# Performance work log

Hardware: AMD Instinct MI355X
Metric: run time of the kernel (lower is better)

## Reference

```python
import jax, jax.numpy as jnp
import numpy as np

VAR0, VAR1 = 0.1, 0.2   # cfg['variance']
THRESH = 0.5            # overlap_thresh
THETA = 0.01
NEGPOS = 3


def decode(loc, priors):
    # priors center-form [P,4]; returns point-form boxes [P,4]
    cxcy = priors[:, :2] + loc[:, :2] * VAR0 * priors[:, 2:]
    wh = priors[:, 2:] * jnp.exp(loc[:, 2:] * VAR1)
    return jnp.concatenate([cxcy - wh * 0.5, cxcy + wh * 0.5], axis=1)


def center_size(b):
    return jnp.concatenate([(b[:, :2] + b[:, 2:]) * 0.5, b[:, 2:] - b[:, :2]], axis=1)


def encode(matched, priors_c):
    # matched point-form [P,4], priors_c center-form [P,4]
    g_cxcy = ((matched[:, :2] + matched[:, 2:]) * 0.5 - priors_c[:, :2]) / (VAR0 * priors_c[:, 2:])
    g_wh = jnp.log((matched[:, 2:] - matched[:, :2]) / priors_c[:, 2:]) / VAR1
    return jnp.concatenate([g_cxcy, g_wh], axis=1)


def jaccard(a, b):
    # a [G,4], b [P,4] point form -> IoU [G,P]
    lt = jnp.maximum(a[:, None, :2], b[None, :, :2])
    rb = jnp.minimum(a[:, None, 2:], b[None, :, 2:])
    wh = jnp.clip(rb - lt, 0.0)
    inter = wh[..., 0] * wh[..., 1]
    area_a = ((a[:, 2] - a[:, 0]) * (a[:, 3] - a[:, 1]))[:, None]
    area_b = ((b[:, 2] - b[:, 0]) * (b[:, 3] - b[:, 1]))[None, :]
    return inter / (area_a + area_b - inter)


def _match_one(truths, labels, gt_mask, arm_loc, priors):
    # refine_match with arm_loc (use_ARM=True path)
    P = priors.shape[0]
    G = truths.shape[0]
    dec = decode(arm_loc, priors)                                 # [P,4]
    ov = jnp.where(gt_mask[:, None], jaccard(truths, dec), -1.0)  # [G,P], padded GT masked out
    best_prior_idx = jnp.argmax(ov, axis=1)                       # [G]
    best_truth_ov = jnp.max(ov, axis=0)                           # [P]
    best_truth_idx = jnp.argmax(ov, axis=0)                       # [P]
    safe = jnp.where(gt_mask, best_prior_idx, P)                  # OOB index -> dropped scatter
    best_truth_ov = best_truth_ov.at[safe].set(2.0, mode='drop')  # force-match each valid GT
    best_truth_idx = best_truth_idx.at[safe].set(jnp.arange(G), mode='drop')
    matched = truths[best_truth_idx]                              # [P,4]
    conf = jnp.where(best_truth_ov < THRESH, 0, labels[best_truth_idx])
    loc = encode(matched, center_size(dec))
    return loc, conf


def forward(arm_loc, arm_conf, odm_loc, odm_conf, priors, targets, num_gts):
    B, P, C = odm_conf.shape
    truths = targets[..., :4]
    labels = targets[..., 4].astype(jnp.int32)
    gt_mask = jnp.arange(targets.shape[1])[None, :] < num_gts[:, None]
    loc_t, conf_t = jax.vmap(_match_one, in_axes=(0, 0, 0, 0, None))(
        truths, labels, gt_mask,
        jax.lax.stop_gradient(arm_loc), jax.lax.stop_gradient(priors))
    loc_t = jax.lax.stop_gradient(loc_t)    # loc_t.requires_grad = False
    conf_t = jax.lax.stop_gradient(conf_t)

    # ARM objectness filter on positives
    p_obj = jax.nn.softmax(arm_conf, axis=2)[:, :, 1]
    pos = (conf_t > 0) & (p_obj > THETA)

    # masked smooth-L1 localization loss (sum)
    posf = pos[..., None].astype(odm_loc.dtype)
    d = jnp.abs(odm_loc * posf - loc_t * posf)
    loss_l = jnp.sum(jnp.where(d < 1.0, 0.5 * d * d, d - 0.5))

    # hard negative mining on per-prior softmax loss
    batch_conf = odm_conf.reshape(-1, C)
    lc = jax.nn.logsumexp(batch_conf, axis=1) - jnp.take_along_axis(
        batch_conf, conf_t.reshape(-1, 1), axis=1)[:, 0]
    lc = jnp.where(pos.reshape(-1), 0.0, lc).reshape(B, P)
    loss_idx = jnp.argsort(-lc, axis=1)
    idx_rank = jnp.argsort(loss_idx, axis=1)
    num_pos = jnp.sum(pos.astype(jnp.int32), axis=1, keepdims=True)  # [B,1]
    num_neg = jnp.minimum(NEGPOS * num_pos, P - 1)
    neg = idx_rank < num_neg
    mask = pos | neg

    # masked cross entropy (compute on zeroed-out logits like the original, then mask)
    conf_p = (odm_conf * mask[..., None].astype(odm_conf.dtype)).reshape(-1, C)
    tgt = jnp.where(mask, conf_t, 0).reshape(-1)
    logp = jax.nn.log_softmax(conf_p, axis=1)
    ce = -jnp.take_along_axis(logp, tgt[:, None], axis=1)[:, 0]
    loss_c = jnp.sum(ce * mask.reshape(-1).astype(ce.dtype))

    N = jnp.sum(num_pos).astype(jnp.float32)
    return loss_l / N, loss_c / N


def setup_inputs():
    key = jax.random.key(0)
    ks = jax.random.split(key, 10)
    B, P, C, G = 32, 16320, 21, 40
    arm_loc = jax.random.normal(ks[0], (B, P, 4), jnp.float32) * 0.1
    arm_conf = jax.random.normal(ks[1], (B, P, 2), jnp.float32)
    odm_loc = jax.random.normal(ks[2], (B, P, 4), jnp.float32) * 0.1
    odm_conf = jax.random.normal(ks[3], (B, P, C), jnp.float32)
    # priors in center form with positive sizes
    pc = jax.random.uniform(ks[4], (P, 2), jnp.float32, 0.1, 0.9)
    pwh = jax.random.uniform(ks[5], (P, 2), jnp.float32, 0.05, 0.3)
    priors = jnp.concatenate([pc, pwh], axis=1)
    # GT boxes in point form with positive area, labels in 1..C-1, padded to G=40
    gc = jax.random.uniform(ks[6], (B, G, 2), jnp.float32, 0.2, 0.8)
    gwh = jax.random.uniform(ks[7], (B, G, 2), jnp.float32, 0.05, 0.3)
    boxes = jnp.concatenate([gc - gwh * 0.5, gc + gwh * 0.5], axis=-1)
    labels = jax.random.randint(ks[8], (B, G, 1), 1, C).astype(jnp.float32)
    targets = jnp.concatenate([boxes, labels], axis=-1)
    num_gts = jax.random.randint(ks[9], (B,), 1, G + 1).astype(jnp.int32)
    return {"arm_loc": arm_loc, "arm_conf": arm_conf, "odm_loc": odm_loc,
            "odm_conf": odm_conf, "priors": priors, "targets": targets,
            "num_gts": num_gts}


def reference(arm_loc, arm_conf, odm_loc, odm_conf, priors, targets, num_gts):
    return forward(arm_loc, arm_conf, odm_loc, odm_conf, priors, targets, num_gts)
```

## Files before the change

### kernel.cpp

```cpp
#include <hip/hip_runtime.h>
#include <math.h>

#define VAR0 0.1f
#define VAR1 0.2f
#define THRESH 0.5f
#define THETA 0.01f
#define MAXG 64
#define BLK 256
#define SELT 1024
#define NCH 16
#define NB 4096
#define CAP 2048

__device__ __forceinline__ float4 decode_box(float4 l, float4 pr) {
    float cx = pr.x + l.x * VAR0 * pr.z;
    float cy = pr.y + l.y * VAR0 * pr.w;
    float w = pr.z * expf(l.z * VAR1);
    float h = pr.w * expf(l.w * VAR1);
    return make_float4(cx - w * 0.5f, cy - h * 0.5f, cx + w * 0.5f, cy + h * 0.5f);
}

__device__ __forceinline__ float smooth_l1_sum(float4 ol, float4 t, float4 d) {
    float pcx = (d.x + d.z) * 0.5f, pcy = (d.y + d.w) * 0.5f;
    float pw = d.z - d.x, ph = d.w - d.y;
    float g0 = ((t.x + t.z) * 0.5f - pcx) / (VAR0 * pw);
    float g1 = ((t.y + t.w) * 0.5f - pcy) / (VAR0 * ph);
    float g2 = logf((t.z - t.x) / pw) / VAR1;
    float g3 = logf((t.w - t.y) / ph) / VAR1;
    float s = 0.f, dd;
    dd = fabsf(ol.x - g0); s += (dd < 1.f) ? 0.5f*dd*dd : dd - 0.5f;
    dd = fabsf(ol.y - g1); s += (dd < 1.f) ? 0.5f*dd*dd : dd - 0.5f;
    dd = fabsf(ol.z - g2); s += (dd < 1.f) ? 0.5f*dd*dd : dd - 0.5f;
    dd = fabsf(ol.w - g3); s += (dd < 1.f) ? 0.5f*dd*dd : dd - 0.5f;
    return s;
}

__device__ __forceinline__ unsigned wave_umax_bits(unsigned v) {
    int x = (int)v;
    int t;
    t = __builtin_amdgcn_update_dpp(0, x, 0x111, 0xf, 0xf, true);  x = (t > x) ? t : x;
    t = __builtin_amdgcn_update_dpp(0, x, 0x112, 0xf, 0xf, true);  x = (t > x) ? t : x;
    t = __builtin_amdgcn_update_dpp(0, x, 0x114, 0xf, 0xf, true);  x = (t > x) ? t : x;
    t = __builtin_amdgcn_update_dpp(0, x, 0x118, 0xf, 0xf, true);  x = (t > x) ? t : x;
    t = __builtin_amdgcn_update_dpp(0, x, 0x142, 0xa, 0xf, false); x = (t > x) ? t : x;
    t = __builtin_amdgcn_update_dpp(0, x, 0x143, 0xc, 0xf, false); x = (t > x) ? t : x;
    return (unsigned)__builtin_amdgcn_readlane(x, 63);
}

__global__ void k_fused(const float* __restrict__ arm_loc, const float* __restrict__ priors,
                        const float* __restrict__ arm_conf,
                        const float* __restrict__ odm_loc, const float* __restrict__ odm_conf,
                        const float* __restrict__ targets, const int* __restrict__ num_gts,
                        float* __restrict__ ce, unsigned char* __restrict__ posm,
                        unsigned* __restrict__ bb,
                        unsigned long long* __restrict__ bpw,
                        float* __restrict__ partL, int* __restrict__ partN,
                        int B, int P, int C, int G) {
    int b = blockIdx.y;
    int p0 = blockIdx.x * BLK;
    int tid = threadIdx.x;
    int p = p0 + tid;
    int lane = tid & 63, wid = tid >> 6;
    int wavebase = p0 + (tid & ~63);
    __shared__ float4 st4[MAXG];
    __shared__ float  stl[MAXG];
    __shared__ float  sarea[MAXG];
    __shared__ unsigned long long wk[4][MAXG];
    __shared__ float oc_s[BLK * 21];
    __shared__ int sng;
    if (tid == 0) sng = num_gts[b];
    for (int g = tid; g < G; g += BLK) {
        const float* tg = targets + (size_t)b * G * 5 + g * 5;
        float t0 = tg[0], t1 = tg[1], t2 = tg[2], t3 = tg[3];
        st4[g] = make_float4(t0, t1, t2, t3);
        stl[g] = tg[4];
        sarea[g] = (t2 - t0) * (t3 - t1);
    }
    int nrows = P - p0; if (nrows > BLK) nrows = BLK;
    int nf = nrows * C;
    const float* ocb = odm_conf + ((size_t)b * P + p0) * C;
    int nf4 = nf >> 2;
    const float4* ocb4 = (const float4*)ocb;
    for (int i2 = tid; i2 < nf4; i2 += BLK) ((float4*)oc_s)[i2] = ocb4[i2];
    if (tid < (nf & 3)) oc_s[(nf4 << 2) + tid] = ocb[(nf4 << 2) + tid];
    __syncthreads();
    int ng = sng;
    bool ok = p < P;
    float4 d = make_float4(0.f, 0.f, 0.f, 0.f);
    float areaB = 0.f;
    size_t i = (size_t)b * P + (ok ? p : 0);
    if (ok) {
        float4 l = ((const float4*)arm_loc)[i];
        float4 pr = ((const float4*)priors)[p];
        d = decode_box(l, pr);
        areaB = (d.z - d.x) * (d.w - d.y);
    }
    float bov = -2.0f; int bidx = 0;
    for (int g = 0; g < ng; ++g) {
        float4 t = st4[g];
        unsigned vbits = 0u;
        if (ok) {
            float lt0 = fmaxf(t.x, d.x), lt1 = fmaxf(t.y, d.y);
            float rb0 = fminf(t.z, d.z), rb1 = fminf(t.w, d.w);
            float w = rb0 - lt0; if (w < 0.f) w = 0.f;
            float h = rb1 - lt1; if (h < 0.f) h = 0.f;
            float inter = w * h;
            float ov = inter / (sarea[g] + areaB - inter);
            if (ov > bov) { bov = ov; bidx = g; }
            vbits = __float_as_uint(ov);
        }
        unsigned om = wave_umax_bits(vbits);
        unsigned long long mask = __ballot(ok && vbits == om);
        if (lane == 0) {
            unsigned long long key = 0ull;
            if (mask) {
                int p_win = wavebase + (int)__builtin_ctzll(mask);
                key = ((unsigned long long)om << 32)
                    | (unsigned long long)(0xFFFFFFFFu - (unsigned)p_win);
            }
            wk[wid][g] = key;
        }
    }
    float lsum = 0.f; int pc = 0;
    if (ok) {
        int conf_t = (bov < THRESH) ? 0 : (int)stl[bidx];
        float2 c = ((const float2*)arm_conf)[i];
        float mm = fmaxf(c.x, c.y);
        float e0 = expf(c.x - mm), e1 = expf(c.y - mm);
        float p_obj = e1 / (e0 + e1);
        bool pos = (conf_t > 0) && (p_obj > THETA);
        if (pos) {
            pc = 1;
            float4 ol = ((const float4*)odm_loc)[i];
            lsum = smooth_l1_sum(ol, st4[bidx], d);
        }
        const float* oc = oc_s + tid * C;
        float mx = oc[0];
        for (int j = 1; j < C; ++j) mx = fmaxf(mx, oc[j]);
        float sume = 0.f;
        for (int j = 0; j < C; ++j) sume += expf(oc[j] - mx);
        float lse = mx + logf(sume);
        float cev = lse - oc[conf_t];
        ce[i] = cev;
        posm[i] = pos ? 1 : 0;
        bb[i] = (__float_as_uint(bov) & 0xFFFFFFC0u) | (unsigned)bidx;
    }
    __shared__ float rl[BLK];
    __shared__ int rc[BLK];
    rl[tid] = lsum; rc[tid] = pc;
    __syncthreads();
    if (tid < ng) {
        unsigned long long k0 = wk[0][tid], k1 = wk[1][tid];
        unsigned long long k2 = wk[2][tid], k3 = wk[3][tid];
        unsigned long long m01 = k0 > k1 ? k0 : k1;
        unsigned long long m23 = k2 > k3 ? k2 : k3;
        unsigned long long m = m01 > m23 ? m01 : m23;
        bpw[(size_t)(b * G + tid) * gridDim.x + blockIdx.x] = m;
    }
    for (int off = BLK/2; off > 0; off >>= 1) {
        if (tid < off) { rl[tid] += rl[tid+off]; rc[tid] += rc[tid+off]; }
        __syncthreads();
    }
    if (tid == 0) {
        partL[b * gridDim.x + blockIdx.x] = rl[0];
        partN[b * gridDim.x + blockIdx.x] = rc[0];
    }
}

__global__ __launch_bounds__(1024) void k_fixpatch(
        const float* __restrict__ arm_loc, const float* __restrict__ priors,
        const float* __restrict__ arm_conf, const float* __restrict__ odm_loc,
        const float* __restrict__ odm_conf,
        const float* __restrict__ targets, const int* __restrict__ num_gts,
        const unsigned long long* __restrict__ bpw, const unsigned* __restrict__ bb,
        float* __restrict__ ce, unsigned char* __restrict__ posm,
        float* __restrict__ partPL, int* __restrict__ partPN,
        int B, int P, int C, int G, int NBX) {
    int b = blockIdx.x;
    int tid = threadIdx.x;
    int lane = tid & 63, wid = tid >> 6;
    __shared__ int fp[MAXG];
    __shared__ float4 st4[MAXG];
    __shared__ float  stl[MAXG];
    __shared__ int sng;
    if (tid == 0) sng = num_gts[b];
    for (int g = tid; g < G; g += 1024) {
        const float* tg = targets + (size_t)b * G * 5 + g * 5;
        st4[g] = make_float4(tg[0], tg[1], tg[2], tg[3]);
        stl[g] = tg[4];
    }
    __syncthreads();
    int ng = sng;
    for (int g = wid; g < ng; g += 16) {
        const unsigned long long* src = bpw + (size_t)(b * G + g) * NBX;
        unsigned long long key = 0ull;
        for (int j = lane; j < NBX; j += 64) {
            unsigned long long v = src[j];
            if (v > key) key = v;
        }
        for (int off = 32; off > 0; off >>= 1) {
            unsigned long long o = __shfl_down(key, (unsigned)off, 64);
            if (o > key) key = o;
        }
        if (lane == 0) fp[g] = (int)(0xFFFFFFFFu - (unsigned)(key & 0xFFFFFFFFull));
    }
    __syncthreads();
    if (tid < G) {
        float dL = 0.f; int dN = 0;
        if (tid < ng) {
            int g = tid;
            bool dup = false;
            for (int g2 = g + 1; g2 < ng; ++g2) if (fp[g2] == fp[g]) { dup = true; break; }
            if (!dup) {
                int p = fp[g];
                size_t i = (size_t)b * P + p;
                unsigned bbv = bb[i];
                int old_bidx = (int)(bbv & 63u);
                bool old_ge = __uint_as_float(bbv & 0xFFFFFFC0u) >= THRESH;
                int old_ct = old_ge ? (int)stl[old_bidx] : 0;
                int new_ct = (int)stl[g];
                float2 c = ((const float2*)arm_conf)[i];
                float mm = fmaxf(c.x, c.y);
                float e0 = expf(c.x - mm), e1 = expf(c.y - mm);
                float p_obj = e1 / (e0 + e1);
                bool old_pos = (old_ct > 0) && (p_obj > THETA);
                bool new_pos = (p_obj > THETA);
                if (old_pos || new_pos) {
                    float4 l = ((const float4*)arm_loc)[i];
                    float4 pr = ((const float4*)priors)[p];
                    float4 d = decode_box(l, pr);
                    float4 ol = ((const float4*)odm_loc)[i];
                    if (old_pos) dL -= smooth_l1_sum(ol, st4[old_bidx], d);
                    if (new_pos) dL += smooth_l1_sum(ol, st4[g], d);
                }
                dN = (new_pos ? 1 : 0) - (old_pos ? 1 : 0);
                const float* oc = odm_conf + i * (size_t)C;
                float ce_old = ce[i];
                float ce_new = (old_ct == new_ct) ? ce_old
                             : (ce_old + oc[old_ct] - oc[new_ct]);
                ce[i] = ce_new;
                posm[i] = new_pos ? 1 : 0;
            }
        }
        partPL[b * G + tid] = dL;
        partPN[b * G + tid] = dN;
    }
}

__global__ __launch_bounds__(SELT) void k_select(
        const float* __restrict__ ce, const unsigned char* __restrict__ posm,
        const int* __restrict__ partN, const int* __restrict__ partPN,
        const float* __restrict__ partL, const float* __restrict__ partPL,
        int NBX, int G,
        float* __restrict__ partC, float* __restrict__ totL,
        int* __restrict__ npos, int P) {
    int b = blockIdx.x;
    int tid = threadIdx.x;
    int lane = tid & 63, wid = tid >> 6;
    __shared__ unsigned hist[NB];
    __shared__ float cv[CAP];
    __shared__ int   ci[CAP];
    __shared__ int   sums[SELT];
    __shared__ int   redi[16];
    __shared__ float redf[16];
    __shared__ int sh_base[16];
    __shared__ int sh_m, sh_b1, sh_k1, sh_npos, sh_istar, sh_kk, sh_cum;
    __shared__ unsigned sh_T, sh_pref;
    __shared__ float sh_mx, sh_totl;

    int c0 = 0; float l0 = 0.f;
    for (int j = tid; j < NBX; j += SELT) { c0 += partN[b * NBX + j]; l0 += partL[b * NBX + j]; }
    for (int g = tid; g < G; g += SELT)   { c0 += partPN[b * G + g];  l0 += partPL[b * G + g]; }
    for (int off = 32; off > 0; off >>= 1) {
        c0 += __shfl_down(c0, (unsigned)off, 64);
        l0 += __shfl_down(l0, (unsigned)off, 64);
    }
    if (lane == 0) { redi[wid] = c0; redf[wid] = l0; }
    __syncthreads();
    if (tid < 64) {
        int v = (tid < 16) ? redi[tid] : 0;
        float f = (tid < 16) ? redf[tid] : 0.f;
        for (int off = 32; off > 0; off >>= 1) {
            v += __shfl_down(v, (unsigned)off, 64);
            f += __shfl_down(f, (unsigned)off, 64);
        }
        if (tid == 0) { sh_npos = v; sh_totl = f; }
    }
    __syncthreads();
    int npos_b = sh_npos;
    long K = 3L * npos_b;
    if (K > P - 1) K = P - 1;

    unsigned cb[NCH];
    unsigned lv[NCH];
    unsigned pmw = 0u;
    const unsigned* ceb = (const unsigned*)ce + (size_t)b * P;
    const unsigned char* pb = posm + (size_t)b * P;
    #pragma unroll
    for (int c = 0; c < NCH; ++c) {
        int i = c * SELT + tid;
        unsigned cbits = (i < P) ? ceb[i] : 0u;
        bool ps = (i < P) && (pb[i] != 0);
        cb[c] = cbits;
        if (ps) pmw |= (1u << c);
        lv[c] = ps ? 0u : cbits;
    }

    unsigned uT = 0xFFFFFFFFu; int istar = -1;
    if (K > 0) {
        float mx = 0.f;
        #pragma unroll
        for (int c = 0; c < NCH; ++c) mx = fmaxf(mx, __uint_as_float(lv[c]));
        for (int off = 32; off > 0; off >>= 1) mx = fmaxf(mx, __shfl_xor(mx, off, 64));
        if (lane == 0) redf[wid] = mx;
        __syncthreads();
        if (tid == 0) {
            float v = redf[0];
            for (int w = 1; w < 16; ++w) v = fmaxf(v, redf[w]);
            sh_mx = v;
        }
        __syncthreads();
        float vmax = sh_mx;
        float scale = (vmax > 0.f) ? ((float)NB / vmax) : 0.f;

        for (int j = tid; j < NB; j += SELT) hist[j] = 0u;
        __syncthreads();
        #pragma unroll
        for (int c = 0; c < NCH; ++c) {
            int i = c * SELT + tid;
            if (i < P) {
                int bn = (int)(__uint_as_float(lv[c]) * scale);
                if (bn > NB - 1) bn = NB - 1;
                atomicAdd(&hist[bn], 1u);
            }
        }
        __syncthreads();

        int s4 = (int)(hist[4*tid] + hist[4*tid+1] + hist[4*tid+2] + hist[4*tid+3]);
        sums[SELT - 1 - tid] = s4;
        __syncthreads();
        int x = sums[tid];
        int xs = x;
        for (int off = 1; off < 64; off <<= 1) {
            int o = __shfl_up(xs, (unsigned)off, 64);
            if (lane >= off) xs += o;
        }
        if (lane == 63) redi[wid] = xs;
        __syncthreads();
        if (tid < 64) {
            int v = (tid < 16) ? redi[tid] : 0;
            int vs = v;
            for (int off = 1; off < 16; off <<= 1) {
                int o = __shfl_up(vs, (unsigned)off, 64);
                if (lane >= off) vs += o;
            }
            if (tid < 16) redi[tid] = vs - v;
        }
        __syncthreads();
        int excl_rev = xs + redi[wid] - x;
        sums[tid] = excl_rev;
        __syncthreads();
        int suf = sums[SELT - 1 - tid];
        {
            int run = suf;
            for (int j = 3; j >= 0; --j) {
                int bin = 4 * tid + j;
                int h = (int)hist[bin];
                if ((long)run < K && K <= (long)run + h) { sh_b1 = bin; sh_k1 = (int)(K - run); }
                run += h;
            }
        }
        __syncthreads();
        int B1 = sh_b1, k1 = sh_k1;

        if (tid == 0) sh_m = 0;
        __syncthreads();
        #pragma unroll
        for (int c = 0; c < NCH; ++c) {
            int i = c * SELT + tid;
            if (i < P) {
                float f = __uint_as_float(lv[c]);
                int bn = (int)(f * scale);
                if (bn > NB - 1) bn = NB - 1;
                if (bn == B1) {
                    int pos = atomicAdd(&sh_m, 1);
                    if (pos < CAP) { cv[pos] = f; ci[pos] = i; }
                }
            }
        }
        __syncthreads();
        int m = sh_m;
        if (m <= CAP) {
            for (int j = tid; j < m; j += SELT) {
                float vj = cv[j]; int ij = ci[j]; int r = 0;
                for (int jj = 0; jj < m; ++jj) {
                    float vx = cv[jj];
                    r += (vx > vj || (vx == vj && ci[jj] < ij)) ? 1 : 0;
                }
                if (r == k1 - 1) { sh_T = __float_as_uint(vj); sh_istar = ij; }
            }
            __syncthreads();
            uT = sh_T; istar = sh_istar;
        } else {
            if (tid == 0) { sh_pref = 0u; sh_kk = (int)K; }
            __syncthreads();
            for (int bit = 30; bit >= 0; --bit) {
                unsigned pref = sh_pref;
                int kk = sh_kk;
                unsigned hi = pref >> (bit + 1);
                int cnt = 0;
                #pragma unroll
                for (int c = 0; c < NCH; ++c) {
                    int i = c * SELT + tid;
                    unsigned v = lv[c];
                    cnt += ((i < P) && ((v >> (bit + 1)) == hi) && ((v >> bit) & 1u)) ? 1 : 0;
                }
                for (int off = 32; off > 0; off >>= 1) cnt += __shfl_down(cnt, (unsigned)off, 64);
                if (lane == 0) redi[wid] = cnt;
                __syncthreads();
                if (tid < 64) {
                    int v = (tid < 16) ? redi[tid] : 0;
                    for (int off = 32; off > 0; off >>= 1) v += __shfl_down(v, (unsigned)off, 64);
                    if (tid == 0) {
                        if (kk <= v) sh_pref = pref | (1u << bit);
                        else sh_kk = kk - v;
                    }
                }
                __syncthreads();
            }
            unsigned T = sh_pref; int krem = sh_kk;
            if (tid == 0) { sh_istar = -1; sh_cum = 0; }
            __syncthreads();
            for (int c = 0; c < NCH; ++c) {
                int i = c * SELT + tid;
                bool eq = (i < P) && (lv[c] == T);
                unsigned long long mk = __ballot(eq);
                if (lane == 0) redi[wid] = (int)__popcll(mk);
                __syncthreads();
                if (tid < 64) {
                    int v = (tid < 16) ? redi[tid] : 0;
                    for (int off = 1; off < 16; off <<= 1) {
                        int o = __shfl_up(v, (unsigned)off, 64);
                        if (lane >= off) v += o;
                    }
                    if (tid < 16) sh_base[tid] = v;
                }
                __syncthreads();
                int cum = sh_cum;
                int base = (wid == 0) ? 0 : sh_base[wid - 1];
                if (eq) {
                    int r = cum + base + (int)__popcll(mk & ((1ull << lane) - 1ull));
                    if (r == krem - 1) sh_istar = i;
                }
                __syncthreads();
                if (tid == 0) sh_cum = cum + sh_base[15];
                __syncthreads();
                if (sh_cum >= krem) break;
            }
            __syncthreads();
            uT = T; istar = sh_istar;
        }
    }

    float cs = 0.f;
    #pragma unroll
    for (int c = 0; c < NCH; ++c) {
        int i = c * SELT + tid;
        if (i < P) {
            unsigned v = lv[c];
            bool sel = ((pmw >> c) & 1u) || (v > uT) || (v == uT && i <= istar);
            if (sel) cs += __uint_as_float(cb[c]);
        }
    }
    for (int off = 32; off > 0; off >>= 1) cs += __shfl_down(cs, (unsigned)off, 64);
    if (lane == 0) redf[wid] = cs;
    __syncthreads();
    if (tid < 64) {
        float v = (tid < 16) ? redf[tid] : 0.f;
        for (int off = 32; off > 0; off >>= 1) v += __shfl_down(v, (unsigned)off, 64);
        if (tid == 0) { partC[b] = v; npos[b] = npos_b; totL[b] = sh_totl; }
    }
}

__global__ void k_final(const float* __restrict__ totL, const float* __restrict__ partC,
                        const int* __restrict__ npos, float* __restrict__ out, int B) {
    int tid = threadIdx.x;
    float aL = (tid < B) ? totL[tid] : 0.f;
    float aC = (tid < B) ? partC[tid] : 0.f;
    int   aN = (tid < B) ? npos[tid] : 0;
    for (int off = 32; off > 0; off >>= 1) {
        aL += __shfl_down(aL, (unsigned)off, 64);
        aC += __shfl_down(aC, (unsigned)off, 64);
        aN += __shfl_down(aN, (unsigned)off, 64);
    }
    if (tid == 0) {
        float N = (float)aN;
        out[0] = aL / N;
        out[1] = aC / N;
    }
}

extern "C" void kernel_launch(void* const* d_in, const int* in_sizes, int n_in,
                              void* d_out, int out_size, void* d_ws, size_t ws_size,
                              hipStream_t stream) {
    const float* arm_loc  = (const float*)d_in[0];
    const float* arm_conf = (const float*)d_in[1];
    const float* odm_loc  = (const float*)d_in[2];
    const float* odm_conf = (const float*)d_in[3];
    const float* priors   = (const float*)d_in[4];
    const float* targets  = (const float*)d_in[5];
    const int*   num_gts  = (const int*)d_in[6];
    float* out = (float*)d_out;

    int B = in_sizes[6];
    int P = in_sizes[4] / 4;
    int C = in_sizes[3] / (B * P);
    int G = in_sizes[5] / (B * 5);
    int NBX = (P + BLK - 1) / BLK;

    char* ws = (char*)d_ws;
    size_t off = 0;
    auto alloc = [&](size_t bytes) -> void* {
        void* ptr = ws + off;
        off = (off + bytes + 255) & ~(size_t)255;
        return ptr;
    };
    unsigned long long* bpw = (unsigned long long*)alloc((size_t)B * G * NBX * 8);
    unsigned* bb = (unsigned*)alloc((size_t)B * P * 4);
    float* ce  = (float*)alloc((size_t)B * P * sizeof(float));
    unsigned char* posm = (unsigned char*)alloc((size_t)B * P);
    float* partL = (float*)alloc((size_t)B * NBX * sizeof(float));
    int* partN   = (int*)alloc((size_t)B * NBX * sizeof(int));
    float* partPL = (float*)alloc((size_t)B * G * sizeof(float));
    int* partPN   = (int*)alloc((size_t)B * G * sizeof(int));
    float* partC = (float*)alloc((size_t)B * sizeof(float));
    float* totL  = (float*)alloc((size_t)B * sizeof(float));
    int* npos    = (int*)alloc((size_t)B * sizeof(int));

    k_fused<<<dim3(NBX, B), BLK, 0, stream>>>(arm_loc, priors, arm_conf, odm_loc, odm_conf,
                                              targets, num_gts, ce, posm, bb, bpw,
                                              partL, partN, B, P, C, G);
    k_fixpatch<<<B, 1024, 0, stream>>>(arm_loc, priors, arm_conf, odm_loc, odm_conf,
                                       targets, num_gts, bpw, bb, ce, posm,
                                       partPL, partPN, B, P, C, G, NBX);
    k_select<<<B, SELT, 0, stream>>>(ce, posm, partN, partPN, partL, partPL,
                                     NBX, G, partC, totL, npos, P);
    k_final<<<1, 64, 0, stream>>>(totL, partC, npos, out, B);
}
```

Baseline: 65.73 us.

## Split fused match kernel into match and LSE kernels, use fast math intrinsics

The fused kernel is split in two. k_match handles IoU matching and the per-wave argmax with its shared memory footprint cut down. A new k_lse kernel stages the odm_conf tile in LDS and computes the cross-entropy, reading the match result back from bb. The GT loop is unrolled by two so the two DPP reductions can interleave, and exp/log/div are replaced with fast intrinsics. The goal is higher occupancy in the matching kernel, paid for with an extra launch, an extra round trip of bb through global memory, and reduced float precision.

```diff
diff --git a/kernel.cpp b/kernel.cpp
--- a/kernel.cpp
+++ b/kernel.cpp
@@ -12,27 +12,44 @@
 #define NB 4096
 #define CAP 2048
 
+__device__ __forceinline__ float fdiv_fast(float a, float b) { return __fdividef(a, b); }
+
 __device__ __forceinline__ float4 decode_box(float4 l, float4 pr) {
     float cx = pr.x + l.x * VAR0 * pr.z;
     float cy = pr.y + l.y * VAR0 * pr.w;
-    float w = pr.z * expf(l.z * VAR1);
-    float h = pr.w * expf(l.w * VAR1);
+    float w = pr.z * __expf(l.z * VAR1);
+    float h = pr.w * __expf(l.w * VAR1);
     return make_float4(cx - w * 0.5f, cy - h * 0.5f, cx + w * 0.5f, cy + h * 0.5f);
 }
 
 __device__ __forceinline__ float smooth_l1_sum(float4 ol, float4 t, float4 d) {
     float pcx = (d.x + d.z) * 0.5f, pcy = (d.y + d.w) * 0.5f;
     float pw = d.z - d.x, ph = d.w - d.y;
-    float g0 = ((t.x + t.z) * 0.5f - pcx) / (VAR0 * pw);
-    float g1 = ((t.y + t.w) * 0.5f - pcy) / (VAR0 * ph);
-    float g2 = logf((t.z - t.x) / pw) / VAR1;
-    float g3 = logf((t.w - t.y) / ph) / VAR1;
+    float g0 = fdiv_fast((t.x + t.z) * 0.5f - pcx, VAR0 * pw);
+    float g1 = fdiv_fast((t.y + t.w) * 0.5f - pcy, VAR0 * ph);
+    float g2 = __logf(fdiv_fast(t.z - t.x, pw)) * (1.0f / VAR1);
+    float g3 = __logf(fdiv_fast(t.w - t.y, ph)) * (1.0f / VAR1);
     float s = 0.f, dd;
     dd = fabsf(ol.x - g0); s += (dd < 1.f) ? 0.5f*dd*dd : dd - 0.5f;
     dd = fabsf(ol.y - g1); s += (dd < 1.f) ? 0.5f*dd*dd : dd - 0.5f;
     dd = fabsf(ol.z - g2); s += (dd < 1.f) ? 0.5f*dd*dd : dd - 0.5f;
     dd = fabsf(ol.w - g3); s += (dd < 1.f) ? 0.5f*dd*dd : dd - 0.5f;
     return s;
+}
+
+__device__ __forceinline__ float softmax_pobj(float2 c) {
+    float mm = fmaxf(c.x, c.y);
+    float e0 = __expf(c.x - mm), e1 = __expf(c.y - mm);
+    return fdiv_fast(e1, e0 + e1);
+}
+
+__device__ __forceinline__ float iou_ov(float4 t, float areaA, float4 d, float areaB) {
+    float lt0 = fmaxf(t.x, d.x), lt1 = fmaxf(t.y, d.y);
+    float rb0 = fminf(t.z, d.z), rb1 = fminf(t.w, d.w);
+    float w = rb0 - lt0; if (w < 0.f) w = 0.f;
+    float h = rb1 - lt1; if (h < 0.f) h = 0.f;
+    float inter = w * h;
+    return fdiv_fast(inter, areaA + areaB - inter);
 }
 
 __device__ __forceinline__ unsigned wave_umax_bits(unsigned v) {
@@ -47,15 +64,14 @@
     return (unsigned)__builtin_amdgcn_readlane(x, 63);
 }
 
-__global__ void k_fused(const float* __restrict__ arm_loc, const float* __restrict__ priors,
-                        const float* __restrict__ arm_conf,
-                        const float* __restrict__ odm_loc, const float* __restrict__ odm_conf,
-                        const float* __restrict__ targets, const int* __restrict__ num_gts,
-                        float* __restrict__ ce, unsigned char* __restrict__ posm,
-                        unsigned* __restrict__ bb,
-                        unsigned long long* __restrict__ bpw,
-                        float* __restrict__ partL, int* __restrict__ partN,
-                        int B, int P, int C, int G) {
+__global__ __launch_bounds__(BLK) void k_match(
+        const float* __restrict__ arm_loc, const float* __restrict__ priors,
+        const float* __restrict__ arm_conf, const float* __restrict__ odm_loc,
+        const float* __restrict__ targets, const int* __restrict__ num_gts,
+        unsigned char* __restrict__ posm, unsigned* __restrict__ bb,
+        unsigned long long* __restrict__ bpw,
+        float* __restrict__ partL, int* __restrict__ partN,
+        int B, int P, int G) {
     int b = blockIdx.y;
     int p0 = blockIdx.x * BLK;
     int tid = threadIdx.x;
@@ -66,7 +82,6 @@
     __shared__ float  stl[MAXG];
     __shared__ float  sarea[MAXG];
     __shared__ unsigned long long wk[4][MAXG];
-    __shared__ float oc_s[BLK * 21];
     __shared__ int sng;
     if (tid == 0) sng = num_gts[b];
     for (int g = tid; g < G; g += BLK) {
@@ -76,13 +91,6 @@
         stl[g] = tg[4];
         sarea[g] = (t2 - t0) * (t3 - t1);
     }
-    int nrows = P - p0; if (nrows > BLK) nrows = BLK;
-    int nf = nrows * C;
-    const float* ocb = odm_conf + ((size_t)b * P + p0) * C;
-    int nf4 = nf >> 2;
-    const float4* ocb4 = (const float4*)ocb;
-    for (int i2 = tid; i2 < nf4; i2 += BLK) ((float4*)oc_s)[i2] = ocb4[i2];
-    if (tid < (nf & 3)) oc_s[(nf4 << 2) + tid] = ocb[(nf4 << 2) + tid];
     __syncthreads();
     int ng = sng;
     bool ok = p < P;
@@ -96,52 +104,68 @@
         areaB = (d.z - d.x) * (d.w - d.y);
     }
     float bov = -2.0f; int bidx = 0;
-    for (int g = 0; g < ng; ++g) {
-        float4 t = st4[g];
-        unsigned vbits = 0u;
+    int g = 0;
+    for (; g + 2 <= ng; g += 2) {
+        float4 t0g = st4[g], t1g = st4[g + 1];
+        unsigned vb0 = 0u, vb1 = 0u;
         if (ok) {
-            float lt0 = fmaxf(t.x, d.x), lt1 = fmaxf(t.y, d.y);
-            float rb0 = fminf(t.z, d.z), rb1 = fminf(t.w, d.w);
-            float w = rb0 - lt0; if (w < 0.f) w = 0.f;
-            float h = rb1 - lt1; if (h < 0.f) h = 0.f;
-            float inter = w * h;
-            float ov = inter / (sarea[g] + areaB - inter);
+            float ov0 = iou_ov(t0g, sarea[g], d, areaB);
+            float ov1 = iou_ov(t1g, sarea[g + 1], d, areaB);
+            if (ov0 > bov) { bov = ov0; bidx = g; }
+            if (ov1 > bov) { bov = ov1; bidx = g + 1; }
+            vb0 = __float_as_uint(ov0);
+            vb1 = __float_as_uint(ov1);
+        }
+        unsigned om0 = wave_umax_bits(vb0);
+        unsigned om1 = wave_umax_bits(vb1);
+        unsigned long long m0 = __ballot(ok && vb0 == om0);
+        unsigned long long m1 = __ballot(ok && vb1 == om1);
+        if (lane == 0) {
+            unsigned long long k0 = 0ull, k1 = 0ull;
+            if (m0) {
+                int pw = wavebase + (int)__builtin_ctzll(m0);
+                k0 = ((unsigned long long)om0 << 32)
+                   | (unsigned long long)(0xFFFFFFFFu - (unsigned)pw);
+            }
+            if (m1) {
+                int pw = wavebase + (int)__builtin_ctzll(m1);
+                k1 = ((unsigned long long)om1 << 32)
+                   | (unsigned long long)(0xFFFFFFFFu - (unsigned)pw);
+            }
+            wk[wid][g] = k0;
+            wk[wid][g + 1] = k1;
+        }
+    }
+    if (g < ng) {
+        float4 tg = st4[g];
+        unsigned vb = 0u;
+        if (ok) {
+            float ov = iou_ov(tg, sarea[g], d, areaB);
             if (ov > bov) { bov = ov; bidx = g; }
-            vbits = __float_as_uint(ov);
-        }
-        unsigned om = wave_umax_bits(vbits);
-        unsigned long long mask = __ballot(ok && vbits == om);
+            vb = __float_as_uint(ov);
+        }
+        unsigned om = wave_umax_bits(vb);
+        unsigned long long m = __ballot(ok && vb == om);
         if (lane == 0) {
-            unsigned long long key = 0ull;
-            if (mask) {
-                int p_win = wavebase + (int)__builtin_ctzll(mask);
-                key = ((unsigned long long)om << 32)
-                    | (unsigned long long)(0xFFFFFFFFu - (unsigned)p_win);
-            }
-            wk[wid][g] = key;
+            unsigned long long k0 = 0ull;
+            if (m) {
+                int pw = wavebase + (int)__builtin_ctzll(m);
+                k0 = ((unsigned long long)om << 32)
+                   | (unsigned long long)(0xFFFFFFFFu - (unsigned)pw);
+            }
+            wk[wid][g] = k0;
         }
     }
     float lsum = 0.f; int pc = 0;
     if (ok) {
         int conf_t = (bov < THRESH) ? 0 : (int)stl[bidx];
-        float2 c = ((const float2*)arm_conf)[i];
-        float mm = fmaxf(c.x, c.y);
-        float e0 = expf(c.x - mm), e1 = expf(c.y - mm);
-        float p_obj = e1 / (e0 + e1);
+        float p_obj = softmax_pobj(((const float2*)arm_conf)[i]);
         bool pos = (conf_t > 0) && (p_obj > THETA);
         if (pos) {
             pc = 1;
             float4 ol = ((const float4*)odm_loc)[i];
             lsum = smooth_l1_sum(ol, st4[bidx], d);
         }
-        const float* oc = oc_s + tid * C;
-        float mx = oc[0];
-        for (int j = 1; j < C; ++j) mx = fmaxf(mx, oc[j]);
-        float sume = 0.f;
-        for (int j = 0; j < C; ++j) sume += expf(oc[j] - mx);
-        float lse = mx + logf(sume);
-        float cev = lse - oc[conf_t];
-        ce[i] = cev;
         posm[i] = pos ? 1 : 0;
         bb[i] = (__float_as_uint(bov) & 0xFFFFFFC0u) | (unsigned)bidx;
     }
@@ -164,6 +188,40 @@
     if (tid == 0) {
         partL[b * gridDim.x + blockIdx.x] = rl[0];
         partN[b * gridDim.x + blockIdx.x] = rc[0];
+    }
+}
+
+__global__ __launch_bounds__(BLK) void k_lse(
+        const float* __restrict__ odm_conf, const float* __restrict__ targets,
+        const unsigned* __restrict__ bb,
+        float* __restrict__ ce, int B, int P, int C, int G) {
+    int b = blockIdx.y;
+    int p0 = blockIdx.x * BLK;
+    int tid = threadIdx.x;
+    int p = p0 + tid;
+    __shared__ float stl[MAXG];
+    __shared__ float oc_s[BLK * 21];
+    for (int gg = tid; gg < G; gg += BLK) stl[gg] = targets[(size_t)b * G * 5 + gg * 5 + 4];
+    int nrows = P - p0; if (nrows > BLK) nrows = BLK;
+    int nf = nrows * C;
+    const float* ocb = odm_conf + ((size_t)b * P + p0) * C;
+    int nf4 = nf >> 2;
+    const float4* ocb4 = (const float4*)ocb;
+    for (int i2 = tid; i2 < nf4; i2 += BLK) ((float4*)oc_s)[i2] = ocb4[i2];
+    if (tid < (nf & 3)) oc_s[(nf4 << 2) + tid] = ocb[(nf4 << 2) + tid];
+    __syncthreads();
+    if (p < P) {
+        size_t i = (size_t)b * P + p;
+        unsigned bbv = bb[i];
+        int bidx = (int)(bbv & 63u);
+        int conf_t = (__uint_as_float(bbv & 0xFFFFFFC0u) >= THRESH) ? (int)stl[bidx] : 0;
+        const float* oc = oc_s + tid * C;
+        float mx = oc[0];
+        for (int j = 1; j < C; ++j) mx = fmaxf(mx, oc[j]);
+        float sume = 0.f;
+        for (int j = 0; j < C; ++j) sume += __expf(oc[j] - mx);
+        float lse = mx + __logf(sume);
+        ce[i] = lse - oc[conf_t];
     }
 }
 
@@ -219,10 +277,7 @@
                 bool old_ge = __uint_as_float(bbv & 0xFFFFFFC0u) >= THRESH;
                 int old_ct = old_ge ? (int)stl[old_bidx] : 0;
                 int new_ct = (int)stl[g];
-                float2 c = ((const float2*)arm_conf)[i];
-                float mm = fmaxf(c.x, c.y);
-                float e0 = expf(c.x - mm), e1 = expf(c.y - mm);
-                float p_obj = e1 / (e0 + e1);
+                float p_obj = softmax_pobj(((const float2*)arm_conf)[i]);
                 bool old_pos = (old_ct > 0) && (p_obj > THETA);
                 bool new_pos = (p_obj > THETA);
                 if (old_pos || new_pos) {
@@ -537,9 +592,9 @@
     float* totL  = (float*)alloc((size_t)B * sizeof(float));
     int* npos    = (int*)alloc((size_t)B * sizeof(int));
 
-    k_fused<<<dim3(NBX, B), BLK, 0, stream>>>(arm_loc, priors, arm_conf, odm_loc, odm_conf,
-                                              targets, num_gts, ce, posm, bb, bpw,
-                                              partL, partN, B, P, C, G);
+    k_match<<<dim3(NBX, B), BLK, 0, stream>>>(arm_loc, priors, arm_conf, odm_loc, targets,
+                                              num_gts, posm, bb, bpw, partL, partN, B, P, G);
+    k_lse<<<dim3(NBX, B), BLK, 0, stream>>>(odm_conf, targets, bb, ce, B, P, C, G);
     k_fixpatch<<<B, 1024, 0, stream>>>(arm_loc, priors, arm_conf, odm_loc, odm_conf,
                                        targets, num_gts, bpw, bb, ce, posm,
                                        partPL, partPN, B, P, C, G, NBX);
```

Result: no change. 64.53 us (-1.8%).
